# Performance work log

Hardware: AMD Instinct MI355X
Metric: run time of the kernel (lower is better)

Reference implementation:

```python
import jax, jax.numpy as jnp
import numpy as np

B, N = 2, 8192


def setup_inputs() -> dict:
    key = jax.random.key(0)
    ks = jax.random.split(key, 12)
    p = lambda k: jax.random.normal(k, (1, 1), jnp.float32) * 0.5
    return {
        "x": jax.random.normal(ks[0], (B, N), jnp.float32),
        "DSM": jax.random.uniform(ks[1], (N, N), jnp.float32),
        "w1": p(ks[2]), "b1": jnp.zeros((1,), jnp.float32),
        "lw1": p(ks[3]), "lb1": jnp.zeros((1,), jnp.float32),
        "lw2": p(ks[4]), "lb2": jnp.zeros((1,), jnp.float32),
        "w2": p(ks[5]), "b2": jnp.zeros((1,), jnp.float32),
        "w3": p(ks[6]), "b3": jnp.zeros((1,), jnp.float32),
        "wa": p(ks[7]), "ba": jnp.zeros((1,), jnp.float32),
        "wv": p(ks[8]), "bv": jnp.zeros((1,), jnp.float32),
    }


def _gcn_weighted(h, adj, w, b):
    # PyG GCNConv(normalize=True) on a complete graph whose edge weights are
    # adj[src, dst]; all self-loops already exist, so add_remaining_self_loops
    # is a no-op. deg[c] = sum over incoming edge weights (column sum),
    # norm[r,c] = deg[r]^-1/2 * adj[r,c] * deg[c]^-1/2, scatter-add at targets.
    deg = jnp.sum(adj, axis=0)                              # [N]
    dinv = jnp.where(deg > 0, jax.lax.rsqrt(deg), 0.0)
    anorm = dinv[:, None] * adj * dinv[None, :]             # [src, dst]
    hw = h * w[0, 0]                                        # Linear(1,1,bias=False)
    out = jnp.einsum('rc,brd->bcd', anorm, hw)              # [B,N,1]
    return out + b


def _gcn_uniform(h, w, b):
    # edge_weight=None on the complete graph: deg = N everywhere, every
    # normalized edge weight = 1/N -> output at each node is the node-mean.
    m = jnp.mean(h * w[0, 0], axis=-2, keepdims=True)       # [B,1,1]
    return jnp.broadcast_to(m, h.shape) + b


def reference(x, DSM, w1, b1, lw1, lb1, lw2, lb2, w2, b2, w3, b3, wa, ba, wv, bv):
    h = x[:, :, None]                                       # [B,N,1]
    h = jax.nn.relu(_gcn_weighted(h, DSM, w1, b1))
    h = jax.nn.relu(h * lw1[0, 0] + lb1)
    h = jax.nn.relu(h * lw2[0, 0] + lb2)
    h = jax.nn.relu(_gcn_uniform(h, w2, b2))
    h = jax.nn.relu(_gcn_uniform(h, w3, b3))
    action_prob = jax.nn.softmax(h * wa[0, 0] + ba, axis=-1)  # [B,N,1]
    u = jnp.max(h, axis=0, keepdims=True)                   # MaxAggregation dim=0
    v = jnp.max(u, axis=-2, keepdims=True)                  # MaxAggregation dim=-2
    state_values = v * wv[0, 0] + bv                        # [1,1,1]
    return action_prob, state_values
```

## Files before the change

kernel.cpp:

```cpp
#include <hip/hip_runtime.h>
#include <math.h>

#define N 8192
#define NV4 (N / 4)
#define RPB 64
#define NBY (N / RPB)
#define GRID_X 8
#define THREADS 256

#define DEGP_OFF  0
#define TPART_OFF (NBY * N)
#define HPART_OFF (TPART_OFF + NBY * 2 * N)

__global__ void k_colsum(const float* __restrict__ dsm, float* __restrict__ degp) {
    int chunk = (blockIdx.x + blockIdx.y) & (GRID_X - 1);
    int c4 = chunk * THREADS + threadIdx.x;
    int r0 = blockIdx.y * RPB;
    const float4* p = (const float4*)dsm;
    float4 acc = {0.f, 0.f, 0.f, 0.f};
#pragma unroll 16
    for (int i = 0; i < RPB; ++i) {
        float4 v = p[(size_t)(r0 + i) * NV4 + c4];
        acc.x += v.x; acc.y += v.y; acc.z += v.z; acc.w += v.w;
    }
    ((float4*)(degp + (size_t)blockIdx.y * N))[c4] = acc;
}

__global__ void k_matvec(const float* __restrict__ dsm, const float* __restrict__ degp,
                         const float* __restrict__ x, float* __restrict__ tpart) {
    __shared__ float sred[4 * RPB];
    __shared__ float sg0[RPB];
    __shared__ float sg1[RPB];
    int r0 = blockIdx.y * RPB;

    {
        int rl = threadIdx.x & 63;
        int q  = threadIdx.x >> 6;
        const float* dp = degp + r0 + rl;
        float s = 0.f;
#pragma unroll 8
        for (int j = 0; j < 32; ++j) s += dp[(size_t)(q * 32 + j) * N];
        sred[q * RPB + rl] = s;
    }
    __syncthreads();
    if (threadIdx.x < RPB) {
        int r = threadIdx.x;
        float d = sred[r] + sred[RPB + r] + sred[2 * RPB + r] + sred[3 * RPB + r];
        float di = d > 0.f ? rsqrtf(d) : 0.f;
        sg0[r] = di * x[r0 + r];
        sg1[r] = di * x[N + r0 + r];
    }
    __syncthreads();

    int chunk = (blockIdx.x + blockIdx.y) & (GRID_X - 1);
    int c4 = chunk * THREADS + threadIdx.x;
    const float4* p = (const float4*)dsm;
    float4 a0 = {0.f, 0.f, 0.f, 0.f};
    float4 a1 = {0.f, 0.f, 0.f, 0.f};
#pragma unroll 16
    for (int i = 0; i < RPB; ++i) {
        float4 v = p[(size_t)(r0 + i) * NV4 + c4];
        float g0 = sg0[i], g1 = sg1[i];
        a0.x += v.x * g0; a0.y += v.y * g0; a0.z += v.z * g0; a0.w += v.w * g0;
        a1.x += v.x * g1; a1.y += v.y * g1; a1.z += v.z * g1; a1.w += v.w * g1;
    }
    ((float4*)(tpart + ((size_t)blockIdx.y * 2 + 0) * N))[c4] = a0;
    ((float4*)(tpart + ((size_t)blockIdx.y * 2 + 1) * N))[c4] = a1;
}

__global__ void k_head(const float* __restrict__ degp, const float* __restrict__ tpart,
                       const float* __restrict__ w1, const float* __restrict__ b1,
                       const float* __restrict__ lw1, const float* __restrict__ lb1,
                       const float* __restrict__ lw2, const float* __restrict__ lb2,
                       float* __restrict__ hpart, float* __restrict__ out) {
    __shared__ float swred[8];
    int c = blockIdx.x * THREADS + threadIdx.x;

    float d = 0.f, t0 = 0.f, t1 = 0.f;
#pragma unroll 8
    for (int by = 0; by < NBY; ++by) {
        d  += degp[(size_t)by * N + c];
        t0 += tpart[((size_t)by * 2 + 0) * N + c];
        t1 += tpart[((size_t)by * 2 + 1) * N + c];
    }
    float di = d > 0.f ? rsqrtf(d) : 0.f;

    float W1 = w1[0], B1 = b1[0];
    float LW1 = lw1[0], LB1 = lb1[0];
    float LW2 = lw2[0], LB2 = lb2[0];
    float h0 = fmaxf(W1 * di * t0 + B1, 0.f);
    h0 = fmaxf(h0 * LW1 + LB1, 0.f);
    h0 = fmaxf(h0 * LW2 + LB2, 0.f);
    float h1 = fmaxf(W1 * di * t1 + B1, 0.f);
    h1 = fmaxf(h1 * LW1 + LB1, 0.f);
    h1 = fmaxf(h1 * LW2 + LB2, 0.f);

    out[c] = 1.0f;
    out[N + c] = 1.0f;

    float v0 = h0, v1 = h1;
    for (int off = 32; off > 0; off >>= 1) {
        v0 += __shfl_down(v0, off);
        v1 += __shfl_down(v1, off);
    }
    int wave = threadIdx.x >> 6;
    if ((threadIdx.x & 63) == 0) { swred[wave] = v0; swred[4 + wave] = v1; }
    __syncthreads();
    if (threadIdx.x == 0) {
        hpart[blockIdx.x * 2 + 0] = swred[0] + swred[1] + swred[2] + swred[3];
        hpart[blockIdx.x * 2 + 1] = swred[4] + swred[5] + swred[6] + swred[7];
    }
}

__global__ void k_out(const float* __restrict__ hpart,
                      const float* __restrict__ w2, const float* __restrict__ b2,
                      const float* __restrict__ w3, const float* __restrict__ b3,
                      const float* __restrict__ wv, const float* __restrict__ bv,
                      float* __restrict__ out) {
    int tid = threadIdx.x;
    float s0 = tid < 32 ? hpart[tid * 2 + 0] : 0.f;
    float s1 = tid < 32 ? hpart[tid * 2 + 1] : 0.f;
    for (int off = 16; off > 0; off >>= 1) {
        s0 += __shfl_down(s0, off);
        s1 += __shfl_down(s1, off);
    }
    if (tid == 0) {
        float vmax = -INFINITY;
        float m0 = s0 * (1.0f / (float)N);
        float m1 = s1 * (1.0f / (float)N);
        float a = fmaxf(m0 * w2[0] + b2[0], 0.f);
        a = fmaxf(a * w3[0] + b3[0], 0.f);
        float b = fmaxf(m1 * w2[0] + b2[0], 0.f);
        b = fmaxf(b * w3[0] + b3[0], 0.f);
        vmax = fmaxf(a, b);
        out[2 * N] = vmax * wv[0] + bv[0];
    }
}

extern "C" void kernel_launch(void* const* d_in, const int* in_sizes, int n_in,
                              void* d_out, int out_size, void* d_ws, size_t ws_size,
                              hipStream_t stream) {
    const float* x   = (const float*)d_in[0];
    const float* dsm = (const float*)d_in[1];
    const float* w1  = (const float*)d_in[2];
    const float* b1  = (const float*)d_in[3];
    const float* lw1 = (const float*)d_in[4];
    const float* lb1 = (const float*)d_in[5];
    const float* lw2 = (const float*)d_in[6];
    const float* lb2 = (const float*)d_in[7];
    const float* w2  = (const float*)d_in[8];
    const float* b2  = (const float*)d_in[9];
    const float* w3  = (const float*)d_in[10];
    const float* b3  = (const float*)d_in[11];
    const float* wv  = (const float*)d_in[14];
    const float* bv  = (const float*)d_in[15];

    float* ws    = (float*)d_ws;
    float* degp  = ws + DEGP_OFF;
    float* tpart = ws + TPART_OFF;
    float* hpart = ws + HPART_OFF;

    dim3 big(GRID_X, NBY);
    k_colsum<<<big, THREADS, 0, stream>>>(dsm, degp);
    k_matvec<<<big, THREADS, 0, stream>>>(dsm, degp, x, tpart);
    k_head<<<N / THREADS, THREADS, 0, stream>>>(degp, tpart, w1, b1, lw1, lb1,
                                                lw2, lb2, hpart, (float*)d_out);
    k_out<<<1, 64, 0, stream>>>(hpart, w2, b2, w3, b3, wv, bv, (float*)d_out);
}
```

Measured before the change: 439.5 us.

## Split colsum and matvec passes into halves ordered for cache reuse

The column-sum pass now runs as two launches over the left and right column halves. The matvec pass runs as two launches over the bottom and top row halves, with the bottom half first. The order is meant to let the matvec start on matrix data that the previous launch read recently and may still be in the large last-level cache, cutting HBM traffic on the second full read of the 256MB matrix. Each launch now has half as many blocks, and the extra launches add per-launch and tail overhead.

```diff
diff --git a/kernel.cpp b/kernel.cpp
--- a/kernel.cpp
+++ b/kernel.cpp
@@ -3,18 +3,19 @@
 
 #define N 8192
 #define NV4 (N / 4)
+#define HV4 (NV4 / 2)
 #define RPB 64
-#define NBY (N / RPB)
-#define GRID_X 8
+#define NST (N / RPB)
 #define THREADS 256
 
 #define DEGP_OFF  0
-#define TPART_OFF (NBY * N)
-#define HPART_OFF (TPART_OFF + NBY * 2 * N)
+#define TPART_OFF (NST * N)
+#define HPART_OFF (TPART_OFF + NST * 2 * N)
 
-__global__ void k_colsum(const float* __restrict__ dsm, float* __restrict__ degp) {
-    int chunk = (blockIdx.x + blockIdx.y) & (GRID_X - 1);
-    int c4 = chunk * THREADS + threadIdx.x;
+__global__ void k_colsum(const float* __restrict__ dsm, float* __restrict__ degp,
+                         int c4_base) {
+    int chunk = (blockIdx.x + blockIdx.y) & 3;
+    int c4 = c4_base + chunk * THREADS + threadIdx.x;
     int r0 = blockIdx.y * RPB;
     const float4* p = (const float4*)dsm;
     float4 acc = {0.f, 0.f, 0.f, 0.f};
@@ -27,11 +28,13 @@
 }
 
 __global__ void k_matvec(const float* __restrict__ dsm, const float* __restrict__ degp,
-                         const float* __restrict__ x, float* __restrict__ tpart) {
+                         const float* __restrict__ x, float* __restrict__ tpart,
+                         int r_base) {
     __shared__ float sred[4 * RPB];
     __shared__ float sg0[RPB];
     __shared__ float sg1[RPB];
-    int r0 = blockIdx.y * RPB;
+    int r0 = r_base + blockIdx.y * RPB;
+    int gst = r0 / RPB;
 
     {
         int rl = threadIdx.x & 63;
@@ -52,7 +55,7 @@
     }
     __syncthreads();
 
-    int chunk = (blockIdx.x + blockIdx.y) & (GRID_X - 1);
+    int chunk = (blockIdx.x + blockIdx.y) & 7;
     int c4 = chunk * THREADS + threadIdx.x;
     const float4* p = (const float4*)dsm;
     float4 a0 = {0.f, 0.f, 0.f, 0.f};
@@ -64,8 +67,8 @@
         a0.x += v.x * g0; a0.y += v.y * g0; a0.z += v.z * g0; a0.w += v.w * g0;
         a1.x += v.x * g1; a1.y += v.y * g1; a1.z += v.z * g1; a1.w += v.w * g1;
     }
-    ((float4*)(tpart + ((size_t)blockIdx.y * 2 + 0) * N))[c4] = a0;
-    ((float4*)(tpart + ((size_t)blockIdx.y * 2 + 1) * N))[c4] = a1;
+    ((float4*)(tpart + ((size_t)gst * 2 + 0) * N))[c4] = a0;
+    ((float4*)(tpart + ((size_t)gst * 2 + 1) * N))[c4] = a1;
 }
 
 __global__ void k_head(const float* __restrict__ degp, const float* __restrict__ tpart,
@@ -78,10 +81,10 @@
 
     float d = 0.f, t0 = 0.f, t1 = 0.f;
 #pragma unroll 8
-    for (int by = 0; by < NBY; ++by) {
-        d  += degp[(size_t)by * N + c];
-        t0 += tpart[((size_t)by * 2 + 0) * N + c];
-        t1 += tpart[((size_t)by * 2 + 1) * N + c];
+    for (int st = 0; st < NST; ++st) {
+        d  += degp[(size_t)st * N + c];
+        t0 += tpart[((size_t)st * 2 + 0) * N + c];
+        t1 += tpart[((size_t)st * 2 + 1) * N + c];
     }
     float di = d > 0.f ? rsqrtf(d) : 0.f;
 
@@ -125,15 +128,13 @@
         s1 += __shfl_down(s1, off);
     }
     if (tid == 0) {
-        float vmax = -INFINITY;
         float m0 = s0 * (1.0f / (float)N);
         float m1 = s1 * (1.0f / (float)N);
         float a = fmaxf(m0 * w2[0] + b2[0], 0.f);
         a = fmaxf(a * w3[0] + b3[0], 0.f);
         float b = fmaxf(m1 * w2[0] + b2[0], 0.f);
         b = fmaxf(b * w3[0] + b3[0], 0.f);
-        vmax = fmaxf(a, b);
-        out[2 * N] = vmax * wv[0] + bv[0];
+        out[2 * N] = fmaxf(a, b) * wv[0] + bv[0];
     }
 }
 
@@ -160,9 +161,12 @@
     float* tpart = ws + TPART_OFF;
     float* hpart = ws + HPART_OFF;
 
-    dim3 big(GRID_X, NBY);
-    k_colsum<<<big, THREADS, 0, stream>>>(dsm, degp);
-    k_matvec<<<big, THREADS, 0, stream>>>(dsm, degp, x, tpart);
+    dim3 gC(4, NST);
+    dim3 gM(8, NST / 2);
+    k_colsum<<<gC, THREADS, 0, stream>>>(dsm, degp, 0);
+    k_colsum<<<gC, THREADS, 0, stream>>>(dsm, degp, HV4);
+    k_matvec<<<gM, THREADS, 0, stream>>>(dsm, degp, x, tpart, N / 2);
+    k_matvec<<<gM, THREADS, 0, stream>>>(dsm, degp, x, tpart, 0);
     k_head<<<N / THREADS, THREADS, 0, stream>>>(degp, tpart, w1, b1, lw1, lb1,
                                                 lw2, lb2, hpart, (float*)d_out);
     k_out<<<1, 64, 0, stream>>>(hpart, w2, b2, w3, b3, wv, bv, (float*)d_out);
```

Result: slower. 448.8 us (+2.1%).
